# Kernel optimization log

Hardware: AMD Instinct MI355X
Metric: run time of the kernel (lower is better)

Reference implementation:

```python
import jax, jax.numpy as jnp
import numpy as np

# Loss hyperparameters (from init_kwargs defaults)
ALPHA, BETA, GAMMA = 1.0, 2.0, 1.0
DAY_W, NIGHT_W = 2.0, 0.5
PEAK_WIN_W, PEAK_WIN = 3.0, 2
HIGH_POWER_W, POWER_PCT = 1.5, 0.75
HOURS = 24

B, S = 4096, 4032  # seq_len = 24 * 168 days


def setup_inputs() -> dict:
    key = jax.random.key(0)
    k1, k2 = jax.random.split(key)
    y_true = jax.random.uniform(k1, (B, S), dtype=jnp.float32)
    # predictions = truth + noise, clipped to be realistic power values
    y_pred = y_true + 0.1 * jax.random.normal(k2, (B, S), dtype=jnp.float32)
    return {"y_pred": y_pred, "y_true": y_true}


def _daily_peaks(y, day_mask):
    # y, day_mask: (B, D, H). Peaks restricted to daytime hours.
    masked = jnp.where(day_mask, y, jnp.float32(-1e9))
    times = jnp.argmax(masked, axis=-1)                                   # (B, D) int
    vals = jnp.take_along_axis(y, times[..., None], axis=-1)[..., 0]      # (B, D)
    return times, vals


def reference(y_pred, y_true):
    b, s = y_true.shape
    d = s // HOURS
    # default is_daytime: hour-of-day in [6, 20]
    hour = jnp.arange(HOURS, dtype=jnp.int32)
    day_hour_mask = (hour >= 6) & (hour <= 20)                            # (H,)
    is_daytime = jnp.broadcast_to(day_hour_mask[None, None, :], (b, d, HOURS))

    yt = y_true.reshape(b, d, HOURS)
    yp = y_pred.reshape(b, d, HOURS)

    true_times, true_peaks = _daily_peaks(yt, is_daytime)
    pred_times, pred_peaks = _daily_peaks(yp, is_daytime)
    peak_time_errors = (pred_times - true_times).astype(jnp.float32)      # (B, D)

    # --- step weights: day/night base, x PEAK_WIN_W in [peak-2, peak+2] ---
    base_w = jnp.where(is_daytime, jnp.float32(DAY_W), jnp.float32(NIGHT_W))  # (B,D,H)
    pt = true_times[..., None]                                            # (B,D,1)
    in_window = (hour[None, None, :] >= pt - PEAK_WIN) & (hour[None, None, :] <= pt + PEAK_WIN)
    step_w = base_w * jnp.where(in_window, jnp.float32(PEAK_WIN_W), jnp.float32(1.0))
    step_w = step_w.reshape(b, s)

    sq_err = (y_pred - y_true) ** 2
    L_overall = jnp.sum(sq_err * step_w) / jnp.sum(step_w)

    # --- peak magnitude loss with high-power sample weighting ---
    sample_avg_peaks = jnp.mean(true_peaks, axis=1)                       # (B,)
    thr = jnp.quantile(sample_avg_peaks, POWER_PCT)
    high = sample_avg_peaks > thr                                         # (B,) bool
    sample_w = jnp.where(high[:, None], jnp.float32(HIGH_POWER_W), jnp.float32(1.0))
    sample_w = jnp.broadcast_to(sample_w, true_peaks.shape)               # (B, D)
    peak_sq = (pred_peaks - true_peaks) ** 2
    L_peak_mag = jnp.sum(peak_sq * sample_w) / jnp.sum(sample_w)

    L_peak_timing = jnp.mean(jnp.abs(peak_time_errors) * 10.0)

    return ALPHA * L_overall + BETA * L_peak_mag + GAMMA * L_peak_timing
```

## Files before the change

### kernel.cpp

```cpp
#include <hip/hip_runtime.h>
#include <math.h>

#define S_LEN   4032
#define HOURS   24
#define DAYS    168
#define DPB     42
#define ACT     252
#define QPB     4
#define NB_MAX  4096


__global__ __launch_bounds__(256, 8) void day_kernel(
    const float* __restrict__ y_pred, const float* __restrict__ y_true,
    float* __restrict__ SEp, float* __restrict__ SWp, float* __restrict__ Tp,
    float* __restrict__ Pp, float* __restrict__ Ap)
{
    __shared__ float s_tv[ACT], s_pv[ACT];
    __shared__ int   s_th[ACT], s_ph[ACT];
    __shared__ int   s_tt[DPB];
    __shared__ float s_red[5][4];

    const int tid = threadIdx.x;
    const int lane = tid & 63;
    const int wv = tid >> 6;

    float se = 0.f, sw = 0.f, ap = 0.f, pp = 0.f, tp = 0.f;

    float yp[4], yt[4];
    int j = tid % 6;
    int dl = tid / 6;

    if (tid < ACT) {
        const size_t base = (size_t)blockIdx.x * (DPB * HOURS) + (size_t)tid * 4;
        float4 p4 = *(const float4*)(y_pred + base);
        float4 t4 = *(const float4*)(y_true + base);
        yp[0] = p4.x; yp[1] = p4.y; yp[2] = p4.z; yp[3] = p4.w;
        yt[0] = t4.x; yt[1] = t4.y; yt[2] = t4.z; yt[3] = t4.w;

        float tv = -1e30f, pv = -1e30f; int th = 0, ph = 0;
#pragma unroll
        for (int k = 0; k < 4; ++k) {
            int h = 4 * j + k;
            bool day = (h >= 6) && (h <= 20);
            if (day && yt[k] > tv) { tv = yt[k]; th = h; }
            if (day && yp[k] > pv) { pv = yp[k]; ph = h; }
        }
        s_tv[tid] = tv; s_th[tid] = th;
        s_pv[tid] = pv; s_ph[tid] = ph;
    }
    __syncthreads();

    if (tid < DPB) {
        int o = tid * 6;
        float tb = s_tv[o]; int tt = s_th[o];
        float pb = s_pv[o]; int pt = s_ph[o];
#pragma unroll
        for (int jj = 1; jj < 6; ++jj) {
            float v = s_tv[o + jj];
            if (v > tb) { tb = v; tt = s_th[o + jj]; }
            float w = s_pv[o + jj];
            if (w > pb) { pb = w; pt = s_ph[o + jj]; }
        }
        s_tt[tid] = tt;
        ap = tb;
        float dp = pb - tb;
        pp = dp * dp;
        tp = fabsf((float)(pt - tt));
    }
    __syncthreads();

    if (tid < ACT) {
        int tt = s_tt[dl];
#pragma unroll
        for (int k = 0; k < 4; ++k) {
            int h = 4 * j + k;
            bool day = (h >= 6) && (h <= 20);
            float bw = day ? 2.0f : 0.5f;
            float w = bw * (((h >= tt - 2) && (h <= tt + 2)) ? 3.0f : 1.0f);
            float d = yp[k] - yt[k];
            se = fmaf(d * d, w, se);
            sw += w;
        }
    }

    float vals[5] = {se, sw, ap, pp, tp};
#pragma unroll
    for (int q = 0; q < 5; ++q) {
        float v = vals[q];
#pragma unroll
        for (int o = 32; o > 0; o >>= 1) v += __shfl_down(v, o, 64);
        if (lane == 0) s_red[q][wv] = v;
    }
    __syncthreads();
    if (tid == 0) {
        SEp[blockIdx.x] = s_red[0][0] + s_red[0][1] + s_red[0][2] + s_red[0][3];
        SWp[blockIdx.x] = s_red[1][0] + s_red[1][1] + s_red[1][2] + s_red[1][3];
        Ap[blockIdx.x]  = s_red[2][0] + s_red[2][1] + s_red[2][2] + s_red[2][3];
        Pp[blockIdx.x]  = s_red[3][0] + s_red[3][1] + s_red[3][2] + s_red[3][3];
        Tp[blockIdx.x]  = s_red[4][0] + s_red[4][1] + s_red[4][2] + s_red[4][3];
    }
}


__global__ __launch_bounds__(256) void rank_kernel(
    const float* __restrict__ Ap, float* __restrict__ A_out,
    float* __restrict__ qout, int nB)
{
    __shared__ float sA[NB_MAX];
    const int tid = threadIdx.x;

    for (int i = tid; i < nB; i += 256) {
        float4 p = *(const float4*)(Ap + 4 * i);
        float a = (p.x + p.y + p.z + p.w) * (1.0f / (float)DAYS);
        sA[i] = a;
        if (blockIdx.x == 0) A_out[i] = a;
    }
    __syncthreads();

    const int b = blockIdx.x * 128 + (tid >> 1);
    const int half = tid & 1;
    if (b >= nB) return;
    const float v = sA[b];
    const int span = nB / 2;
    const float4* s4 = (const float4*)(sA + half * span);

    int cl = 0, ce = 0;
    for (int i = 0; i < span / 4; ++i) {
        float4 x = s4[i];
        cl += (x.x < v) + (x.y < v) + (x.z < v) + (x.w < v);
        ce += (x.x == v) + (x.y == v) + (x.z == v) + (x.w == v);
    }
    cl += __shfl_xor(cl, 1, 64);
    ce += __shfl_xor(ce, 1, 64);

    if (half == 0) {
        double pos = 0.75 * (double)(nB - 1);
        int lo = (int)pos;
        int hi = (lo + 1 < nB) ? lo + 1 : lo;
        if (lo >= cl && lo < cl + ce) qout[0] = v;
        if (hi >= cl && hi < cl + ce) qout[1] = v;
    }
}


__device__ inline double block_reduce_d(double v, double* scratch, int tid) {
#pragma unroll
    for (int o = 32; o > 0; o >>= 1) v += __shfl_down(v, o, 64);
    if ((tid & 63) == 0) scratch[tid >> 6] = v;
    __syncthreads();
    double r = 0.0;
    if (tid == 0) r = scratch[0] + scratch[1] + scratch[2] + scratch[3];
    __syncthreads();
    return r;
}

__global__ __launch_bounds__(256) void final_kernel(
    const float* __restrict__ SEp, const float* __restrict__ SWp,
    const float* __restrict__ Tp, const float* __restrict__ Pp,
    const float* __restrict__ A, const float* __restrict__ qout,
    float* __restrict__ out, int nB)
{
    __shared__ double s_dred[4];
    const int tid = threadIdx.x;
    const int nBlk = nB * QPB;

    double pos = 0.75 * (double)(nB - 1);
    double frac = pos - (double)((int)pos);
    float thr = (float)((double)qout[0] + frac * ((double)qout[1] - (double)qout[0]));

    double se = 0.0, sw = 0.0, te = 0.0, wp = 0.0, wsum = 0.0;
    for (int i = tid; i < nBlk; i += 256) {
        se += (double)SEp[i];
        sw += (double)SWp[i];
        te += (double)Tp[i];
    }
    for (int b = tid; b < nB; b += 256) {
        float4 p = *(const float4*)(Pp + 4 * b);
        float Pb = p.x + p.y + p.z + p.w;
        float w = (A[b] > thr) ? 1.5f : 1.0f;
        wp   += (double)w * (double)Pb;
        wsum += (double)w;
    }
    se   = block_reduce_d(se,   s_dred, tid);
    sw   = block_reduce_d(sw,   s_dred, tid);
    te   = block_reduce_d(te,   s_dred, tid);
    wp   = block_reduce_d(wp,   s_dred, tid);
    wsum = block_reduce_d(wsum, s_dred, tid);

    if (tid == 0) {
        double L_overall = se / sw;
        double L_peak    = wp / ((double)DAYS * wsum);
        double L_timing  = 10.0 * te / ((double)nB * (double)DAYS);
        out[0] = (float)(L_overall + 2.0 * L_peak + L_timing);
    }
}


extern "C" void kernel_launch(void* const* d_in, const int* in_sizes, int n_in,
                              void* d_out, int out_size, void* d_ws, size_t ws_size,
                              hipStream_t stream) {
    const float* y_pred = (const float*)d_in[0];
    const float* y_true = (const float*)d_in[1];
    int total = in_sizes[0];
    int nB = total / S_LEN;
    int nBlk = nB * QPB;

    float* ws  = (float*)d_ws;
    float* SEp = ws;
    float* SWp = ws + 1 * (size_t)nBlk;
    float* Tp  = ws + 2 * (size_t)nBlk;
    float* Pp  = ws + 3 * (size_t)nBlk;
    float* Ap  = ws + 4 * (size_t)nBlk;
    float* A   = ws + 5 * (size_t)nBlk;
    float* q   = ws + 5 * (size_t)nBlk + (size_t)nB;

    day_kernel<<<nBlk, 256, 0, stream>>>(y_pred, y_true, SEp, SWp, Tp, Pp, Ap);
    rank_kernel<<<(nB + 127) / 128, 256, 0, stream>>>(Ap, A, q, nB);
    final_kernel<<<1, 256, 0, stream>>>(SEp, SWp, Tp, Pp, A, q, (float*)d_out, nB);
}
```

Before: 188.2 us.

## Use persistent wave-level day processing with shuffle argmax and register prefetch

Replaces the one-block-per-42-days kernel with a persistent grid in which each wavefront processes 10 days per iteration. The per-day argmax is done with cross-lane shuffles and ballots instead of shared memory and block barriers. The next chunk is loaded into registers before the current one is processed, to overlap memory latency with compute. Per-day peak values go to global memory and are reduced by a new per-sample kernel. This adds a fourth launch and extra global traffic for the per-day arrays, and leaves 4 of every 64 lanes idle.

```diff
diff --git a/kernel.cpp b/kernel.cpp
--- a/kernel.cpp
+++ b/kernel.cpp
@@ -1,120 +1,136 @@
 #include <hip/hip_runtime.h>
 #include <math.h>
 
+#define HOURS   24
+#define DPS     168
 #define S_LEN   4032
-#define HOURS   24
-#define DAYS    168
-#define DPB     42
-#define ACT     252
-#define QPB     4
+#define DPC     10
+#define NBLK    2048
+#define NWAVES  (NBLK * 4)
 #define NB_MAX  4096
 
 
 __global__ __launch_bounds__(256, 8) void day_kernel(
-    const float* __restrict__ y_pred, const float* __restrict__ y_true,
+    const float* __restrict__ yTrue, const float* __restrict__ yPred,
+    float* __restrict__ Aday, float* __restrict__ Pday,
     float* __restrict__ SEp, float* __restrict__ SWp, float* __restrict__ Tp,
-    float* __restrict__ Pp, float* __restrict__ Ap)
-{
-    __shared__ float s_tv[ACT], s_pv[ACT];
-    __shared__ int   s_th[ACT], s_ph[ACT];
-    __shared__ int   s_tt[DPB];
-    __shared__ float s_red[5][4];
-
-    const int tid = threadIdx.x;
-    const int lane = tid & 63;
-    const int wv = tid >> 6;
-
-    float se = 0.f, sw = 0.f, ap = 0.f, pp = 0.f, tp = 0.f;
-
-    float yp[4], yt[4];
-    int j = tid % 6;
-    int dl = tid / 6;
-
-    if (tid < ACT) {
-        const size_t base = (size_t)blockIdx.x * (DPB * HOURS) + (size_t)tid * 4;
-        float4 p4 = *(const float4*)(y_pred + base);
-        float4 t4 = *(const float4*)(y_true + base);
-        yp[0] = p4.x; yp[1] = p4.y; yp[2] = p4.z; yp[3] = p4.w;
-        yt[0] = t4.x; yt[1] = t4.y; yt[2] = t4.z; yt[3] = t4.w;
+    long long totalDays, int nChunks)
+{
+    const int lane = threadIdx.x & 63;
+    const int wIdx = (blockIdx.x << 2) | (threadIdx.x >> 6);
+    const int base = (lane / 6) * 6;
+    const int j    = lane - base;
+    const bool laneActive = (lane < 60);
+
+    float se = 0.f, sw = 0.f, te = 0.f;
+
+    float4 nT = make_float4(0.f, 0.f, 0.f, 0.f);
+    float4 nP = make_float4(0.f, 0.f, 0.f, 0.f);
+    int c = wIdx;
+    if (c < nChunks) {
+        long long d = (long long)c * DPC + (base / 6);
+        bool v = laneActive && (d < totalDays);
+        size_t off = v ? ((size_t)d * HOURS + 4 * j) : 0;
+        nT = *(const float4*)(yTrue + off);
+        nP = *(const float4*)(yPred + off);
+    }
+
+    for (; c < nChunks; c += NWAVES) {
+        float4 cT = nT, cP = nP;
+        int cn = c + NWAVES;
+        if (cn < nChunks) {
+            long long d2 = (long long)cn * DPC + (base / 6);
+            bool v2 = laneActive && (d2 < totalDays);
+            size_t off2 = v2 ? ((size_t)d2 * HOURS + 4 * j) : 0;
+            nT = *(const float4*)(yTrue + off2);
+            nP = *(const float4*)(yPred + off2);
+        }
+
+        const long long d = (long long)c * DPC + (base / 6);
+        const bool valid = laneActive && (d < totalDays);
+
+        float yt[4] = {cT.x, cT.y, cT.z, cT.w};
+        float yp[4] = {cP.x, cP.y, cP.z, cP.w};
 
         float tv = -1e30f, pv = -1e30f; int th = 0, ph = 0;
 #pragma unroll
         for (int k = 0; k < 4; ++k) {
             int h = 4 * j + k;
-            bool day = (h >= 6) && (h <= 20);
-            if (day && yt[k] > tv) { tv = yt[k]; th = h; }
-            if (day && yp[k] > pv) { pv = yp[k]; ph = h; }
+            bool dayh = (h >= 6) && (h <= 20);
+            if (dayh && yt[k] > tv) { tv = yt[k]; th = h; }
+            if (dayh && yp[k] > pv) { pv = yp[k]; ph = h; }
         }
-        s_tv[tid] = tv; s_th[tid] = th;
-        s_pv[tid] = pv; s_ph[tid] = ph;
-    }
-    __syncthreads();
-
-    if (tid < DPB) {
-        int o = tid * 6;
-        float tb = s_tv[o]; int tt = s_th[o];
-        float pb = s_pv[o]; int pt = s_ph[o];
-#pragma unroll
-        for (int jj = 1; jj < 6; ++jj) {
-            float v = s_tv[o + jj];
-            if (v > tb) { tb = v; tt = s_th[o + jj]; }
-            float w = s_pv[o + jj];
-            if (w > pb) { pb = w; pt = s_ph[o + jj]; }
+        if (!valid) { tv = -1e30f; pv = -1e30f; }
+
+        float m1t = fmaxf(tv, __shfl_xor(tv, 1, 64));
+        float m1p = fmaxf(pv, __shfl_xor(pv, 1, 64));
+        float gmt = fmaxf(fmaxf(__shfl(m1t, base, 64), __shfl(m1t, base + 2, 64)),
+                          __shfl(m1t, base + 4, 64));
+        float gmp = fmaxf(fmaxf(__shfl(m1p, base, 64), __shfl(m1p, base + 2, 64)),
+                          __shfl(m1p, base + 4, 64));
+
+        unsigned long long blt = __ballot(valid && (tv == gmt));
+        unsigned long long blp = __ballot(valid && (pv == gmp));
+        int ft = __ffsll(blt >> base) - 1;
+        int fp = __ffsll(blp >> base) - 1;
+        int tt = __shfl(th, base + ft, 64);
+        int pt = __shfl(ph, base + fp, 64);
+
+        if (valid) {
+#pragma unroll
+            for (int k = 0; k < 4; ++k) {
+                int h = 4 * j + k;
+                float bw = ((h >= 6) && (h <= 20)) ? 2.0f : 0.5f;
+                float wgt = bw * (((h >= tt - 2) && (h <= tt + 2)) ? 3.0f : 1.0f);
+                float dd = yp[k] - yt[k];
+                se = fmaf(wgt * dd, dd, se);
+                sw += wgt;
+            }
+            if (j == 0) {
+                te += fabsf((float)(pt - tt));
+                Aday[d] = gmt;
+                float dpk = gmp - gmt;
+                Pday[d] = dpk * dpk;
+            }
         }
-        s_tt[tid] = tt;
-        ap = tb;
-        float dp = pb - tb;
-        pp = dp * dp;
-        tp = fabsf((float)(pt - tt));
-    }
-    __syncthreads();
-
-    if (tid < ACT) {
-        int tt = s_tt[dl];
-#pragma unroll
-        for (int k = 0; k < 4; ++k) {
-            int h = 4 * j + k;
-            bool day = (h >= 6) && (h <= 20);
-            float bw = day ? 2.0f : 0.5f;
-            float w = bw * (((h >= tt - 2) && (h <= tt + 2)) ? 3.0f : 1.0f);
-            float d = yp[k] - yt[k];
-            se = fmaf(d * d, w, se);
-            sw += w;
-        }
-    }
-
-    float vals[5] = {se, sw, ap, pp, tp};
-#pragma unroll
-    for (int q = 0; q < 5; ++q) {
-        float v = vals[q];
-#pragma unroll
-        for (int o = 32; o > 0; o >>= 1) v += __shfl_down(v, o, 64);
-        if (lane == 0) s_red[q][wv] = v;
-    }
-    __syncthreads();
-    if (tid == 0) {
-        SEp[blockIdx.x] = s_red[0][0] + s_red[0][1] + s_red[0][2] + s_red[0][3];
-        SWp[blockIdx.x] = s_red[1][0] + s_red[1][1] + s_red[1][2] + s_red[1][3];
-        Ap[blockIdx.x]  = s_red[2][0] + s_red[2][1] + s_red[2][2] + s_red[2][3];
-        Pp[blockIdx.x]  = s_red[3][0] + s_red[3][1] + s_red[3][2] + s_red[3][3];
-        Tp[blockIdx.x]  = s_red[4][0] + s_red[4][1] + s_red[4][2] + s_red[4][3];
-    }
+    }
+
+#pragma unroll
+    for (int o = 32; o > 0; o >>= 1) {
+        se += __shfl_down(se, o, 64);
+        sw += __shfl_down(sw, o, 64);
+        te += __shfl_down(te, o, 64);
+    }
+    if (lane == 0) { SEp[wIdx] = se; SWp[wIdx] = sw; Tp[wIdx] = te; }
+}
+
+
+__global__ __launch_bounds__(64) void sample_kernel(
+    const float* __restrict__ Aday, const float* __restrict__ Pday,
+    float* __restrict__ A, float* __restrict__ P)
+{
+    const int b = blockIdx.x;
+    const int lane = threadIdx.x;
+    const float* ad = Aday + (size_t)b * DPS;
+    const float* pd = Pday + (size_t)b * DPS;
+    float sa = 0.f, sp = 0.f;
+    for (int i = lane; i < DPS; i += 64) { sa += ad[i]; sp += pd[i]; }
+#pragma unroll
+    for (int o = 32; o > 0; o >>= 1) {
+        sa += __shfl_down(sa, o, 64);
+        sp += __shfl_down(sp, o, 64);
+    }
+    if (lane == 0) { A[b] = sa * (1.0f / (float)DPS); P[b] = sp; }
 }
 
 
 __global__ __launch_bounds__(256) void rank_kernel(
-    const float* __restrict__ Ap, float* __restrict__ A_out,
-    float* __restrict__ qout, int nB)
+    const float* __restrict__ A, float* __restrict__ qout, int nB)
 {
     __shared__ float sA[NB_MAX];
     const int tid = threadIdx.x;
 
-    for (int i = tid; i < nB; i += 256) {
-        float4 p = *(const float4*)(Ap + 4 * i);
-        float a = (p.x + p.y + p.z + p.w) * (1.0f / (float)DAYS);
-        sA[i] = a;
-        if (blockIdx.x == 0) A_out[i] = a;
-    }
+    for (int i = tid; i < nB; i += 256) sA[i] = A[i];
     __syncthreads();
 
     const int b = blockIdx.x * 128 + (tid >> 1);
@@ -156,29 +172,26 @@
 
 __global__ __launch_bounds__(256) void final_kernel(
     const float* __restrict__ SEp, const float* __restrict__ SWp,
-    const float* __restrict__ Tp, const float* __restrict__ Pp,
+    const float* __restrict__ Tp, const float* __restrict__ P,
     const float* __restrict__ A, const float* __restrict__ qout,
-    float* __restrict__ out, int nB)
+    float* __restrict__ out, int nB, int nW)
 {
     __shared__ double s_dred[4];
     const int tid = threadIdx.x;
-    const int nBlk = nB * QPB;
 
     double pos = 0.75 * (double)(nB - 1);
     double frac = pos - (double)((int)pos);
     float thr = (float)((double)qout[0] + frac * ((double)qout[1] - (double)qout[0]));
 
     double se = 0.0, sw = 0.0, te = 0.0, wp = 0.0, wsum = 0.0;
-    for (int i = tid; i < nBlk; i += 256) {
+    for (int i = tid; i < nW; i += 256) {
         se += (double)SEp[i];
         sw += (double)SWp[i];
         te += (double)Tp[i];
     }
     for (int b = tid; b < nB; b += 256) {
-        float4 p = *(const float4*)(Pp + 4 * b);
-        float Pb = p.x + p.y + p.z + p.w;
         float w = (A[b] > thr) ? 1.5f : 1.0f;
-        wp   += (double)w * (double)Pb;
+        wp   += (double)w * (double)P[b];
         wsum += (double)w;
     }
     se   = block_reduce_d(se,   s_dred, tid);
@@ -189,8 +202,8 @@
 
     if (tid == 0) {
         double L_overall = se / sw;
-        double L_peak    = wp / ((double)DAYS * wsum);
-        double L_timing  = 10.0 * te / ((double)nB * (double)DAYS);
+        double L_peak    = wp / ((double)DPS * wsum);
+        double L_timing  = 10.0 * te / ((double)nB * (double)DPS);
         out[0] = (float)(L_overall + 2.0 * L_peak + L_timing);
     }
 }
@@ -203,18 +216,22 @@
     const float* y_true = (const float*)d_in[1];
     int total = in_sizes[0];
     int nB = total / S_LEN;
-    int nBlk = nB * QPB;
-
-    float* ws  = (float*)d_ws;
-    float* SEp = ws;
-    float* SWp = ws + 1 * (size_t)nBlk;
-    float* Tp  = ws + 2 * (size_t)nBlk;
-    float* Pp  = ws + 3 * (size_t)nBlk;
-    float* Ap  = ws + 4 * (size_t)nBlk;
-    float* A   = ws + 5 * (size_t)nBlk;
-    float* q   = ws + 5 * (size_t)nBlk + (size_t)nB;
-
-    day_kernel<<<nBlk, 256, 0, stream>>>(y_pred, y_true, SEp, SWp, Tp, Pp, Ap);
-    rank_kernel<<<(nB + 127) / 128, 256, 0, stream>>>(Ap, A, q, nB);
-    final_kernel<<<1, 256, 0, stream>>>(SEp, SWp, Tp, Pp, A, q, (float*)d_out, nB);
-}
+    long long totalDays = (long long)nB * DPS;
+    int nChunks = (int)((totalDays + DPC - 1) / DPC);
+
+    float* ws   = (float*)d_ws;
+    float* Aday = ws;
+    float* Pday = Aday + (size_t)totalDays;
+    float* SEp  = Pday + (size_t)totalDays;
+    float* SWp  = SEp + NWAVES;
+    float* Tp   = SWp + NWAVES;
+    float* A    = Tp  + NWAVES;
+    float* P    = A   + (size_t)nB;
+    float* q    = P   + (size_t)nB;
+
+    day_kernel<<<NBLK, 256, 0, stream>>>(y_true, y_pred, Aday, Pday, SEp, SWp, Tp,
+                                         totalDays, nChunks);
+    sample_kernel<<<nB, 64, 0, stream>>>(Aday, Pday, A, P);
+    rank_kernel<<<(nB + 127) / 128, 256, 0, stream>>>(A, q, nB);
+    final_kernel<<<1, 256, 0, stream>>>(SEp, SWp, Tp, P, A, q, (float*)d_out, nB, NWAVES);
+}
```

New measurement: 185.9 us. No clear change (-1.2%).
